# Optimization experiments

Hardware: AMD Instinct MI355X
Metric: run time of the kernel (lower is better)

Reference implementation:

```python
import jax, jax.numpy as jnp
from jax import lax
import numpy as np

B, H, W = 8, 96, 96
CIN, COUT, QD, NH = 256, 128, 32, 8
LA_MID = COUT // 8  # 16
GRIDS = (6, 3, 2, 1)
EPS = 1e-5  # torch BatchNorm default eps


def conv2d(x, w):
    # 'same' padding for 3x3 stride 1 (autopad k//2)
    return lax.conv_general_dilated(x, w, (1, 1), 'SAME',
                                    dimension_numbers=('NCHW', 'OIHW', 'NCHW'))


def bn2d(x, g, b, m, v):
    inv = g / jnp.sqrt(v + EPS)
    return x * inv[None, :, None, None] + (b - m * inv)[None, :, None, None]


def adaptive_avg_pool_tokens(x, oh, ow):
    # matches torch adaptive_avg_pool2d bin edges; returns [b, c, oh*ow]
    b, c, h, w = x.shape
    cells = []
    for i in range(oh):
        h0, h1 = (i * h) // oh, -((-(i + 1) * h) // oh)
        for j in range(ow):
            w0, w1 = (j * w) // ow, -((-(j + 1) * w) // ow)
            cells.append(x[:, :, h0:h1, w0:w1].mean(axis=(2, 3)))
    return jnp.stack(cells, axis=-1)


def psp(x, grids):
    b, c, h, w = x.shape
    ar = w / h
    return jnp.concatenate(
        [adaptive_avg_pool_tokens(x, g, max(1, round(ar * g))) for g in grids], axis=2)


def setup_inputs() -> dict:
    key = jax.random.key(0)
    ks = jax.random.split(key, 9)
    f = jnp.float32
    return {
        'x': jax.random.normal(ks[0], (B, CIN, H, W), f),
        'w_red': jax.random.normal(ks[1], (COUT, CIN, 3, 3), f) * 0.02,
        'bng': jnp.ones((COUT,), f), 'bnb': jnp.zeros((COUT,), f),
        'bnm': jnp.zeros((COUT,), f), 'bnv': jnp.ones((COUT,), f),
        'w_q': jax.random.normal(ks[2], (QD, COUT), f) * 0.1,
        'b_q': jnp.zeros((QD,), f),
        'w_k': jax.random.normal(ks[3], (QD, COUT), f) * 0.1,
        'b_k': jnp.zeros((QD,), f),
        'w_v': jax.random.normal(ks[4], (COUT, COUT), f) * 0.08,
        'b_v': jnp.zeros((COUT,), f),
        'lsh': jax.random.normal(ks[5], (NH, QD), f),
        'w_la1': jax.random.normal(ks[6], (LA_MID, COUT), f) * 0.1,
        'lag': jnp.ones((LA_MID,), f), 'lab': jnp.zeros((LA_MID,), f),
        'lam': jnp.zeros((LA_MID,), f), 'lav': jnp.ones((LA_MID,), f),
        'w_la2': jax.random.normal(ks[7], (COUT, LA_MID, 3, 3), f) * 0.02,
    }


def reference(x, w_red, bng, bnb, bnm, bnv, w_q, b_q, w_k, b_k, w_v, b_v,
              lsh, w_la1, lag, lab, lam, lav, w_la2):
    # reduce_channel: Conv(256,128,3) = conv + BN + SiLU
    xr = jax.nn.silu(bn2d(conv2d(x, w_red), bng, bnb, bnm, bnv))  # [B,COUT,H,W]
    b, c, h, w = xr.shape
    # query: 1x1 conv to 32 ch, flatten spatial -> [B, HW, QD]
    q = (jnp.einsum('oc,bchw->bohw', w_q, xr)
         + b_q[None, :, None, None]).reshape(b, QD, h * w).transpose(0, 2, 1)
    # key_psp and value_psp act on the same xr -> identical token sets [B,COUT,50]
    tokens = psp(xr, GRIDS)
    k_tok = (jnp.einsum('oc,bcn->bon', w_k, tokens)
             + b_k[None, :, None]).transpose(0, 2, 1)  # [B,50,QD]
    v_tok = (jnp.einsum('oc,bcn->bon', w_v, tokens)
             + b_v[None, :, None]).transpose(0, 2, 1)  # [B,50,COUT]
    # ReformerAttention: argmax over TOKEN dim -> [B, NH]; sort indices lie in [0,NH)
    # so the gather picks a per-batch permutation of the first NH key/value tokens
    # (faithful to the torch code; q_buckets is computed but unused there).
    k_buckets = jnp.argmax(jnp.einsum('hd,bnd->bhn', lsh, k_tok), axis=-1)  # [B,NH]
    k_idx = jnp.argsort(k_buckets, axis=-1)  # [B,NH], values in [0,NH)
    k_s = jnp.take_along_axis(k_tok, k_idx[:, :, None], axis=1)  # [B,NH,QD]
    v_s = jnp.take_along_axis(v_tok, k_idx[:, :, None], axis=1)  # [B,NH,COUT]
    att = jax.nn.softmax(jnp.einsum('bqd,bkd->bqk', q, k_s), axis=-1)  # [B,HW,NH]
    ctx = jnp.einsum('bqk,bkd->bqd', att, v_s).transpose(0, 2, 1).reshape(b, COUT, h, w)
    # LocalAttenModule: Conv(128,16,1)(conv+bn+silu) -> 3x3 conv 16->128 -> tanh mask
    y = jax.nn.silu(bn2d(jnp.einsum('oc,bchw->bohw', w_la1, ctx), lag, lab, lam, lav))
    mask = jnp.tanh(conv2d(y, w_la2))
    ctx = ctx * mask + ctx
    return xr + ctx
```

## Files before the change

kernel.cpp:

```cpp
#include <hip/hip_runtime.h>
#include <hip/hip_bf16.h>
#include <cmath>

typedef __attribute__((ext_vector_type(8))) short short8;
typedef __attribute__((ext_vector_type(16))) short short16;
typedef __attribute__((ext_vector_type(4))) short s16x4;
typedef __attribute__((ext_vector_type(4))) float f32x4;
typedef __attribute__((ext_vector_type(2))) float f32x2;
typedef unsigned short u16;

#define HW 9216

__device__ inline float bf2f(u16 u) {
    union { unsigned int i; float f; } x; x.i = ((unsigned int)u) << 16; return x.f;
}
__device__ inline u16 f2bf(float f) {
    union { unsigned int i; float f; } x; x.f = f;
    unsigned int r = x.i + 0x7FFF + ((x.i >> 16) & 1);
    return (u16)(r >> 16);
}

__device__ inline void gload16(const u16* g, u16* l) {
    __builtin_amdgcn_global_load_lds(
        (const __attribute__((address_space(1))) void*)g,
        (__attribute__((address_space(3))) void*)l,
        16, 0, 0);
}

__global__ __launch_bounds__(256) void transform_w(
    const float* __restrict__ wred, const float* __restrict__ wla2,
    u16* __restrict__ Wt1, u16* __restrict__ Wt2)
{
    int idx = blockIdx.x * 256 + threadIdx.x;
    if (idx < 128 * 2304) {
        int co = idx / 2304;
        int rem = idx - co * 2304;
        int c = rem / 288;
        int r2 = rem - c * 288;
        int khw = r2 >> 5, ciL = r2 & 31;
        Wt1[idx] = f2bf(wred[((co * 256 + c * 32 + ciL) * 9 + khw)]);
    } else {
        int i2 = idx - 128 * 2304;
        if (i2 < 128 * 160) {
            int co = i2 / 160;
            int k = i2 - co * 160;
            int khw = k >> 4, ci = k & 15;
            Wt2[i2] = (khw < 9) ? f2bf(wla2[((co << 4) + ci) * 9 + khw]) : (u16)0;
        }
    }
}

__global__ __launch_bounds__(256) void transpose_x(
    const float* __restrict__ X, u16* __restrict__ Xt)
{
    int bid = blockIdx.x;
    int b = bid & 7;
    int rem = bid >> 3;
    int chunk = rem % 36;
    int q = rem / 36;
    int p = chunk * 256 + threadIdx.x;
    const float* xb = X + (size_t)b * 256 * HW + p;
    u16* ot = Xt + ((size_t)b * HW + p) * 256;
#pragma unroll
    for (int o2 = 0; o2 < 2; ++o2) {
        int c0 = q * 32 + o2 * 16;
        short16 v;
#pragma unroll
        for (int j = 0; j < 16; ++j)
            v[j] = (short)f2bf(xb[(size_t)(c0 + j) * HW]);
        *(short16*)(ot + c0) = v;
    }
}

template<int CIN, int KTILES, int KP, int EPI>
__global__ __launch_bounds__(256) void conv_k(
    const u16* __restrict__ Xt, const u16* __restrict__ Wt,
    u16* OutH, float* OutF,
    const float* __restrict__ bg, const float* __restrict__ bb,
    const float* __restrict__ bm, const float* __restrict__ bv,
    const u16* __restrict__ xrb, const float* ctxf,
    const u16* __restrict__ zp)
{
    __shared__ __align__(16) short As[2][128 * 32];
    __shared__ __align__(16) short Bs[2][96 * 32];
    __shared__ float invA[128], betA[128];

    const int tid = threadIdx.x;
    const int bid = blockIdx.x;
    const int b = bid & 7;
    const int tile = bid >> 3;
    const int w0 = (tile % 3) * 32;
    const int h0 = (tile / 3) * 3;

    const int lane = tid & 63;
    const int wid = tid >> 6;
    const int wm = (wid & 1) * 64;
    const int wn = (wid >> 1) * 48;
    const int r = lane & 15;
    const int quad = lane >> 4;

    if constexpr (EPI == 1) {
        if (tid < 128) {
            float iv = bg[tid] * rsqrtf(bv[tid] + 1e-5f);
            invA[tid] = iv;
            betA[tid] = bb[tid] - bm[tid] * iv;
        }
    }

    const u16* XtB = Xt + (size_t)b * HW * CIN;

    auto bsrc = [&](int slot, int kt) -> const u16* {
        int row = slot >> 2, o = slot & 3;
        int pw = row & 31, ph = row >> 5;
        int hgl = h0 + ph, wgl = w0 + pw;
        if (CIN == 256) {
            int c = (kt * 57) >> 9;
            int khw = kt - c * 9;
            int dh = (khw * 11) >> 5;
            int dw = khw - 3 * dh;
            int hh = hgl + dh - 1, ww = wgl + dw - 1;
            bool ok = ((unsigned)hh < 96u) && ((unsigned)ww < 96u);
            return ok ? XtB + ((size_t)hh * 96 + ww) * 256 + c * 32 + o * 8 : zp;
        } else {
            int kg = kt * 32 + o * 8;
            int khw = kg >> 4, ci0 = kg & 15;
            int dh = (khw * 11) >> 5, dw = khw - 3 * dh;
            int hh = hgl + dh - 1, ww = wgl + dw - 1;
            bool ok = ((unsigned)hh < 96u) && ((unsigned)ww < 96u) && (khw < 9);
            return ok ? XtB + ((size_t)hh * 96 + ww) * 16 + ci0 : zp;
        }
    };

    auto stage = [&](int kt, int buf) {
        int sA0 = tid, sA1 = tid + 256;
        gload16(Wt + (size_t)(sA0 >> 2) * KP + kt * 32 + (sA0 & 3) * 8,
                (u16*)&As[buf][(64 * wid) * 8]);
        gload16(Wt + (size_t)(sA1 >> 2) * KP + kt * 32 + (sA1 & 3) * 8,
                (u16*)&As[buf][(256 + 64 * wid) * 8]);
        gload16(bsrc(tid, kt), (u16*)&Bs[buf][(64 * wid) * 8]);
        if (wid < 2)
            gload16(bsrc(tid + 256, kt), (u16*)&Bs[buf][(256 + 64 * wid) * 8]);
    };

    f32x4 acc[4][3];
    f32x4 zz = {0.f, 0.f, 0.f, 0.f};
#pragma unroll
    for (int i = 0; i < 4; i++)
#pragma unroll
        for (int j = 0; j < 3; j++) acc[i][j] = zz;

    stage(0, 0);
    __syncthreads();

    for (int kt = 0; kt < KTILES; ++kt) {
        int cur = kt & 1;
        if (kt + 1 < KTILES) stage(kt + 1, cur ^ 1);
        short8 af[4], bfr[3];
#pragma unroll
        for (int i = 0; i < 4; i++)
            af[i] = *(const short8*)(&As[cur][(wm + i * 16 + r) * 32 + quad * 8]);
#pragma unroll
        for (int j = 0; j < 3; j++)
            bfr[j] = *(const short8*)(&Bs[cur][(wn + j * 16 + r) * 32 + quad * 8]);
        __builtin_amdgcn_s_setprio(1);
#pragma unroll
        for (int i = 0; i < 4; i++)
#pragma unroll
            for (int j = 0; j < 3; j++)
                acc[i][j] = __builtin_amdgcn_mfma_f32_16x16x32_bf16(af[i], bfr[j], acc[i][j], 0, 0, 0);
        __builtin_amdgcn_s_setprio(0);
        if (kt + 1 < KTILES)
            __syncthreads();
    }

#pragma unroll
    for (int i = 0; i < 4; i++) {
#pragma unroll
        for (int j = 0; j < 3; j++) {
            int pl = wn + j * 16 + r;
            int w = w0 + (pl & 31), h = h0 + (pl >> 5);
#pragma unroll
            for (int g = 0; g < 4; ++g) {
                int co = wm + i * 16 + quad * 4 + g;
                float v = acc[i][j][g];
                size_t oidx = ((size_t)b * 128 + co) * HW + h * 96 + w;
                if constexpr (EPI == 1) {
                    float val = v * invA[co] + betA[co];
                    float sv = val / (1.f + __expf(-val));
                    OutH[oidx] = f2bf(sv);
                } else {
                    float xv = bf2f(xrb[oidx]);
                    float cv = ctxf[oidx];
                    float e = __expf(2.f * v);
                    float th = 1.f - 2.f / (e + 1.f);
                    OutF[oidx] = xv + cv * (1.f + th);
                }
            }
        }
    }
}

__global__ __launch_bounds__(256) void prep_attn(
    const u16* __restrict__ xr,
    const float* __restrict__ wk, const float* __restrict__ bk,
    const float* __restrict__ wv, const float* __restrict__ bv,
    const float* __restrict__ wq, const float* __restrict__ bq,
    float* __restrict__ Aout, float* __restrict__ Vout, float* __restrict__ c0out)
{
    __shared__ float part[256];
    __shared__ float tok[128];
    __shared__ float ks[32];
    int t = threadIdx.x;
    int bid = blockIdx.x;
    int b = bid & 7, n = bid >> 3;
    int c = t & 127, half = t >> 7;
    int i0 = (n < 6) ? 0 : 16;
    int j0 = ((n < 6) ? n : (n - 6)) * 16;
    const u16* xb = xr + (size_t)(b * 128 + c) * HW;

    float s = 0.f;
    for (int rr = 0; rr < 8; ++rr) {
        int row = i0 + half * 8 + rr;
        const u16* rp = xb + row * 96 + j0;
        short8 v0 = *(const short8*)rp;
        short8 v1 = *(const short8*)(rp + 8);
#pragma unroll
        for (int j = 0; j < 8; ++j) s += bf2f((u16)v0[j]) + bf2f((u16)v1[j]);
    }
    part[t] = s;
    __syncthreads();
    if (t < 128) tok[t] = (part[t] + part[t + 128]) * (1.f / 256.f);
    __syncthreads();
    if (t < 32) {
        float s2 = bk[t];
        for (int cc = 0; cc < 128; ++cc) s2 += wk[t * 128 + cc] * tok[cc];
        ks[t] = s2;
    }
    __syncthreads();
    if (t < 128) {
        float s3 = bv[c];
        for (int c2 = 0; c2 < 128; ++c2) s3 += wv[c * 128 + c2] * tok[c2];
        Vout[((size_t)b * 8 + n) * 128 + c] = s3;
    } else {
        float s4 = 0.f;
        for (int d = 0; d < 32; ++d) s4 += wq[d * 128 + c] * ks[d];
        Aout[((size_t)b * 8 + n) * 128 + c] = s4;
    }
    if (t == 0) {
        float s5 = 0.f;
        for (int d = 0; d < 32; ++d) s5 += bq[d] * ks[d];
        c0out[b * 8 + n] = s5;
    }
}

__global__ __launch_bounds__(256) void attn_k(
    const u16* __restrict__ xr,
    const float* __restrict__ Ain, const float* __restrict__ Vin,
    const float* __restrict__ c0in,
    const float* __restrict__ wla1,
    const float* __restrict__ lag, const float* __restrict__ lab,
    const float* __restrict__ lam, const float* __restrict__ lav,
    float* __restrict__ ctxout, u16* __restrict__ yout)
{
    __shared__ __align__(16) float Xs[128 * 64];
    __shared__ __align__(16) float Ast[128 * 8];
    __shared__ __align__(16) float Vst[128 * 8];
    __shared__ __align__(16) float Wst[128 * 16];
    __shared__ float satt[8 * 64];
    __shared__ float c0s[8], inv1[16], bet1[16];

    int t = threadIdx.x;
    int bid = blockIdx.x;
    int b = bid & 7;
    int p0 = (bid >> 3) * 64;

    for (int i = t; i < 1024; i += 256) {
        int n = i >> 7, c = i & 127;
        Ast[c * 8 + n] = Ain[b * 1024 + i];
        Vst[c * 8 + n] = Vin[b * 1024 + i];
    }
    for (int i = t; i < 2048; i += 256) {
        int d = i >> 7, c = i & 127;
        Wst[c * 16 + d] = wla1[i];
    }
    if (t < 8) c0s[t] = c0in[b * 8 + t];
    if (t < 16) {
        float iv = lag[t] * rsqrtf(lav[t] + 1e-5f);
        inv1[t] = iv; bet1[t] = lab[t] - lam[t] * iv;
    }
    const u16* xb = xr + (size_t)b * 128 * HW + p0;
#pragma unroll
    for (int it = 0; it < 4; ++it) {
        int c = (t >> 3) + it * 32;
        int seg = t & 7;
        short8 v = *(const short8*)(xb + (size_t)c * HW + seg * 8);
        f32x4 f0, f1;
#pragma unroll
        for (int j = 0; j < 4; ++j) { f0[j] = bf2f((u16)v[j]); f1[j] = bf2f((u16)v[j + 4]); }
        *(f32x4*)(&Xs[c * 64 + seg * 8]) = f0;
        *(f32x4*)(&Xs[c * 64 + seg * 8 + 4]) = f1;
    }
    __syncthreads();
    {
        int pp = t & 63, ng = t >> 6;
        float a0 = 0.f, a1 = 0.f;
        for (int c = 0; c < 128; ++c) {
            float x = Xs[c * 64 + pp];
            f32x2 av = *(const f32x2*)(&Ast[c * 8 + ng * 2]);
            a0 += av[0] * x;
            a1 += av[1] * x;
        }
        satt[(ng * 2) * 64 + pp] = a0 + c0s[ng * 2];
        satt[(ng * 2 + 1) * 64 + pp] = a1 + c0s[ng * 2 + 1];
    }
    __syncthreads();
    if (t < 64) {
        float m = -1e30f;
        float sv[8];
#pragma unroll
        for (int n = 0; n < 8; ++n) { sv[n] = satt[n * 64 + t]; m = fmaxf(m, sv[n]); }
        float sum = 0.f;
#pragma unroll
        for (int n = 0; n < 8; ++n) { sv[n] = __expf(sv[n] - m); sum += sv[n]; }
        float rcp = 1.f / sum;
#pragma unroll
        for (int n = 0; n < 8; ++n) satt[n * 64 + t] = sv[n] * rcp;
    }
    __syncthreads();
    {
        int pp = t & 63, cg = t >> 6;
        float at[8];
#pragma unroll
        for (int n = 0; n < 8; ++n) at[n] = satt[n * 64 + pp];
        for (int ci = 0; ci < 32; ++ci) {
            int c = cg * 32 + ci;
            f32x4 v0 = *(const f32x4*)(&Vst[c * 8]);
            f32x4 v1 = *(const f32x4*)(&Vst[c * 8 + 4]);
            float s = at[0] * v0[0] + at[1] * v0[1] + at[2] * v0[2] + at[3] * v0[3]
                    + at[4] * v1[0] + at[5] * v1[1] + at[6] * v1[2] + at[7] * v1[3];
            ctxout[((size_t)b * 128 + c) * HW + p0 + pp] = s;
            Xs[c * 64 + pp] = s;
        }
    }
    __syncthreads();
    {
        int pp = t & 63, dg = t >> 6;
        float a[4] = {0.f, 0.f, 0.f, 0.f};
        for (int c = 0; c < 128; ++c) {
            float x = Xs[c * 64 + pp];
            f32x4 w = *(const f32x4*)(&Wst[c * 16 + dg * 4]);
#pragma unroll
            for (int k = 0; k < 4; ++k) a[k] += w[k] * x;
        }
        s16x4 pk;
#pragma unroll
        for (int k = 0; k < 4; ++k) {
            int d = dg * 4 + k;
            float val = a[k] * inv1[d] + bet1[d];
            float s = val / (1.f + __expf(-val));
            pk[k] = (short)f2bf(s);
        }
        *(s16x4*)(yout + ((size_t)b * HW + p0 + pp) * 16 + dg * 4) = pk;
    }
}

extern "C" void kernel_launch(void* const* d_in, const int* in_sizes, int n_in,
                              void* d_out, int out_size, void* d_ws, size_t ws_size,
                              hipStream_t stream)
{
    const float* x    = (const float*)d_in[0];
    const float* wred = (const float*)d_in[1];
    const float* bng  = (const float*)d_in[2];
    const float* bnb  = (const float*)d_in[3];
    const float* bnm  = (const float*)d_in[4];
    const float* bnv  = (const float*)d_in[5];
    const float* wq   = (const float*)d_in[6];
    const float* bq   = (const float*)d_in[7];
    const float* wk   = (const float*)d_in[8];
    const float* bk   = (const float*)d_in[9];
    const float* wv   = (const float*)d_in[10];
    const float* bv   = (const float*)d_in[11];
    const float* wla1 = (const float*)d_in[13];
    const float* lag  = (const float*)d_in[14];
    const float* lab  = (const float*)d_in[15];
    const float* lam  = (const float*)d_in[16];
    const float* lav  = (const float*)d_in[17];
    const float* wla2 = (const float*)d_in[18];

    char* ws = (char*)d_ws;
    u16*   xr  = (u16*)(ws + 0);
    u16*   yt  = (u16*)(ws + 18874368);
    u16*   Wt1 = (u16*)(ws + 21233664);
    u16*   Wt2 = (u16*)(ws + 21823488);
    float* Ab  = (float*)(ws + 21864448);
    float* Vb  = (float*)(ws + 21897216);
    float* c0b = (float*)(ws + 21929984);
    u16*   xt   = (u16*)d_out;
    float* outp = (float*)d_out;
    const u16* zp = Wt2 + 144;

    transform_w<<<dim3(1232), dim3(256), 0, stream>>>(wred, wla2, Wt1, Wt2);

    transpose_x<<<dim3(2304), dim3(256), 0, stream>>>(x, xt);

    conv_k<256, 72, 2304, 1><<<dim3(768), dim3(256), 0, stream>>>(
        xt, Wt1, xr, nullptr, bng, bnb, bnm, bnv, nullptr, nullptr, zp);

    prep_attn<<<dim3(64), dim3(256), 0, stream>>>(xr, wk, bk, wv, bv, wq, bq, Ab, Vb, c0b);

    attn_k<<<dim3(1152), dim3(256), 0, stream>>>(
        xr, Ab, Vb, c0b, wla1, lag, lab, lam, lav, outp, yt);

    conv_k<16, 5, 160, 2><<<dim3(768), dim3(256), 0, stream>>>(
        yt, Wt2, nullptr, outp, nullptr, nullptr, nullptr, nullptr, xr, outp, zp);
}
```

Before: 289.5 us.

## Fold wla1 into V tokens, tile transpose through LDS, keep attn tile bf16

```diff
diff --git a/kernel.cpp b/kernel.cpp
--- a/kernel.cpp
+++ b/kernel.cpp
@@ -53,22 +53,27 @@
 __global__ __launch_bounds__(256) void transpose_x(
     const float* __restrict__ X, u16* __restrict__ Xt)
 {
+    __shared__ u16 Lt[256][66];
+    int t = threadIdx.x;
     int bid = blockIdx.x;
     int b = bid & 7;
-    int rem = bid >> 3;
-    int chunk = rem % 36;
-    int q = rem / 36;
-    int p = chunk * 256 + threadIdx.x;
-    const float* xb = X + (size_t)b * 256 * HW + p;
-    u16* ot = Xt + ((size_t)b * HW + p) * 256;
-#pragma unroll
-    for (int o2 = 0; o2 < 2; ++o2) {
-        int c0 = q * 32 + o2 * 16;
+    int p0 = (bid >> 3) * 64;
+    int pp = t & 63, c4 = t >> 6;
+    const float* xb = X + (size_t)b * 256 * HW + p0 + pp;
+    for (int r = 0; r < 64; ++r) {
+        int c = r * 4 + c4;
+        Lt[c][pp] = f2bf(xb[(size_t)c * HW]);
+    }
+    __syncthreads();
+    int p = t >> 2, cq = t & 3;
+    u16* ot = Xt + ((size_t)b * HW + p0 + p) * 256 + cq * 64;
+#pragma unroll
+    for (int o = 0; o < 4; ++o) {
         short16 v;
 #pragma unroll
         for (int j = 0; j < 16; ++j)
-            v[j] = (short)f2bf(xb[(size_t)(c0 + j) * HW]);
-        *(short16*)(ot + c0) = v;
+            v[j] = (short)Lt[cq * 64 + o * 16 + j][p];
+        *(short16*)(ot + o * 16) = v;
     }
 }
 
@@ -205,11 +210,14 @@
     const float* __restrict__ wk, const float* __restrict__ bk,
     const float* __restrict__ wv, const float* __restrict__ bv,
     const float* __restrict__ wq, const float* __restrict__ bq,
-    float* __restrict__ Aout, float* __restrict__ Vout, float* __restrict__ c0out)
+    const float* __restrict__ wla1,
+    float* __restrict__ Aout, float* __restrict__ Vout, float* __restrict__ c0out,
+    float* __restrict__ WVout)
 {
     __shared__ float part[256];
     __shared__ float tok[128];
     __shared__ float ks[32];
+    __shared__ float vs[128];
     int t = threadIdx.x;
     int bid = blockIdx.x;
     int b = bid & 7, n = bid >> 3;
@@ -241,6 +249,7 @@
         float s3 = bv[c];
         for (int c2 = 0; c2 < 128; ++c2) s3 += wv[c * 128 + c2] * tok[c2];
         Vout[((size_t)b * 8 + n) * 128 + c] = s3;
+        vs[c] = s3;
     } else {
         float s4 = 0.f;
         for (int d = 0; d < 32; ++d) s4 += wq[d * 128 + c] * ks[d];
@@ -251,21 +260,26 @@
         for (int d = 0; d < 32; ++d) s5 += bq[d] * ks[d];
         c0out[b * 8 + n] = s5;
     }
+    __syncthreads();
+    if (t < 16) {
+        float s6 = 0.f;
+        for (int cc = 0; cc < 128; ++cc) s6 += vs[cc] * wla1[t * 128 + cc];
+        WVout[((size_t)b * 8 + n) * 16 + t] = s6;
+    }
 }
 
 __global__ __launch_bounds__(256) void attn_k(
     const u16* __restrict__ xr,
     const float* __restrict__ Ain, const float* __restrict__ Vin,
-    const float* __restrict__ c0in,
-    const float* __restrict__ wla1,
+    const float* __restrict__ c0in, const float* __restrict__ WVin,
     const float* __restrict__ lag, const float* __restrict__ lab,
     const float* __restrict__ lam, const float* __restrict__ lav,
     float* __restrict__ ctxout, u16* __restrict__ yout)
 {
-    __shared__ __align__(16) float Xs[128 * 64];
+    __shared__ __align__(16) u16 Xh[128 * 64];
     __shared__ __align__(16) float Ast[128 * 8];
     __shared__ __align__(16) float Vst[128 * 8];
-    __shared__ __align__(16) float Wst[128 * 16];
+    __shared__ float WVs[128];
     __shared__ float satt[8 * 64];
     __shared__ float c0s[8], inv1[16], bet1[16];
 
@@ -279,10 +293,7 @@
         Ast[c * 8 + n] = Ain[b * 1024 + i];
         Vst[c * 8 + n] = Vin[b * 1024 + i];
     }
-    for (int i = t; i < 2048; i += 256) {
-        int d = i >> 7, c = i & 127;
-        Wst[c * 16 + d] = wla1[i];
-    }
+    if (t < 128) WVs[t] = WVin[b * 128 + t];
     if (t < 8) c0s[t] = c0in[b * 8 + t];
     if (t < 16) {
         float iv = lag[t] * rsqrtf(lav[t] + 1e-5f);
@@ -294,18 +305,14 @@
         int c = (t >> 3) + it * 32;
         int seg = t & 7;
         short8 v = *(const short8*)(xb + (size_t)c * HW + seg * 8);
-        f32x4 f0, f1;
-#pragma unroll
-        for (int j = 0; j < 4; ++j) { f0[j] = bf2f((u16)v[j]); f1[j] = bf2f((u16)v[j + 4]); }
-        *(f32x4*)(&Xs[c * 64 + seg * 8]) = f0;
-        *(f32x4*)(&Xs[c * 64 + seg * 8 + 4]) = f1;
+        *(short8*)(&Xh[c * 64 + seg * 8]) = v;
     }
     __syncthreads();
     {
         int pp = t & 63, ng = t >> 6;
         float a0 = 0.f, a1 = 0.f;
         for (int c = 0; c < 128; ++c) {
-            float x = Xs[c * 64 + pp];
+            float x = bf2f(Xh[c * 64 + pp]);
             f32x2 av = *(const f32x2*)(&Ast[c * 8 + ng * 2]);
             a0 += av[0] * x;
             a1 += av[1] * x;
@@ -339,28 +346,23 @@
             float s = at[0] * v0[0] + at[1] * v0[1] + at[2] * v0[2] + at[3] * v0[3]
                     + at[4] * v1[0] + at[5] * v1[1] + at[6] * v1[2] + at[7] * v1[3];
             ctxout[((size_t)b * 128 + c) * HW + p0 + pp] = s;
-            Xs[c * 64 + pp] = s;
-        }
-    }
-    __syncthreads();
-    {
-        int pp = t & 63, dg = t >> 6;
+        }
         float a[4] = {0.f, 0.f, 0.f, 0.f};
-        for (int c = 0; c < 128; ++c) {
-            float x = Xs[c * 64 + pp];
-            f32x4 w = *(const f32x4*)(&Wst[c * 16 + dg * 4]);
-#pragma unroll
-            for (int k = 0; k < 4; ++k) a[k] += w[k] * x;
+#pragma unroll
+        for (int n = 0; n < 8; ++n) {
+            f32x4 wv = *(const f32x4*)(&WVs[n * 16 + cg * 4]);
+#pragma unroll
+            for (int k = 0; k < 4; ++k) a[k] += at[n] * wv[k];
         }
         s16x4 pk;
 #pragma unroll
         for (int k = 0; k < 4; ++k) {
-            int d = dg * 4 + k;
+            int d = cg * 4 + k;
             float val = a[k] * inv1[d] + bet1[d];
             float s = val / (1.f + __expf(-val));
             pk[k] = (short)f2bf(s);
         }
-        *(s16x4*)(yout + ((size_t)b * HW + p0 + pp) * 16 + dg * 4) = pk;
+        *(s16x4*)(yout + ((size_t)b * HW + p0 + pp) * 16 + cg * 4) = pk;
     }
 }
 
@@ -395,21 +397,23 @@
     float* Ab  = (float*)(ws + 21864448);
     float* Vb  = (float*)(ws + 21897216);
     float* c0b = (float*)(ws + 21929984);
+    float* WVb = (float*)(ws + 21930240);
     u16*   xt   = (u16*)d_out;
     float* outp = (float*)d_out;
     const u16* zp = Wt2 + 144;
 
     transform_w<<<dim3(1232), dim3(256), 0, stream>>>(wred, wla2, Wt1, Wt2);
 
-    transpose_x<<<dim3(2304), dim3(256), 0, stream>>>(x, xt);
+    transpose_x<<<dim3(1152), dim3(256), 0, stream>>>(x, xt);
 
     conv_k<256, 72, 2304, 1><<<dim3(768), dim3(256), 0, stream>>>(
         xt, Wt1, xr, nullptr, bng, bnb, bnm, bnv, nullptr, nullptr, zp);
 
-    prep_attn<<<dim3(64), dim3(256), 0, stream>>>(xr, wk, bk, wv, bv, wq, bq, Ab, Vb, c0b);
+    prep_attn<<<dim3(64), dim3(256), 0, stream>>>(
+        xr, wk, bk, wv, bv, wq, bq, wla1, Ab, Vb, c0b, WVb);
 
     attn_k<<<dim3(1152), dim3(256), 0, stream>>>(
-        xr, Ab, Vb, c0b, wla1, lag, lab, lam, lav, outp, yt);
+        xr, Ab, Vb, c0b, WVb, lag, lab, lam, lav, outp, yt);
 
     conv_k<16, 5, 160, 2><<<dim3(768), dim3(256), 0, stream>>>(
         yt, Wt2, nullptr, outp, nullptr, nullptr, nullptr, nullptr, xr, outp, zp);
```

Result: faster. 279.2 us (-3.6%).
